# Performance work log

Measured on AMD Instinct MI355X. Metric: run time of the kernel, lower is better.

Reference implementation:

```python
import jax, jax.numpy as jnp
import numpy as np

OUT_F, IN_F = 4096, 11008
NUMEL = OUT_F * IN_F            # divisible by 256
NUM_SUPER = NUMEL // 256        # super-blocks of 8 sub-blocks x 32 values


def setup_inputs() -> dict:
    key = jax.random.key(0)
    k = jax.random.split(key, 7)
    x = jax.random.normal(k[0], (64, IN_F), dtype=jnp.float32)
    packed = jax.random.randint(k[1], (NUMEL // 2,), 0, 256, dtype=jnp.int32)
    d = jax.random.uniform(k[2], (NUM_SUPER,), dtype=jnp.float32) * 0.02
    dmin = jax.random.uniform(k[3], (NUM_SUPER,), dtype=jnp.float32) * 0.02
    scales = jax.random.randint(k[4], (NUM_SUPER * 8,), 0, 64, dtype=jnp.int32)
    mins = jax.random.randint(k[5], (NUM_SUPER * 8,), 0, 64, dtype=jnp.int32)
    bias = jax.random.normal(k[6], (OUT_F,), dtype=jnp.float32) * 0.02
    return {"x": x, "packed": packed, "d": d, "dmin": dmin,
            "scales": scales, "mins": mins, "bias": bias}


def _dequant_q4k(packed, d, dmin, scales, mins):
    # unpack two 4-bit quants per byte, interleaved low/high (stack dim=1 + flatten)
    low = packed & 15
    high = (packed >> 4) & 15
    q = jnp.stack([low, high], axis=1).reshape(NUM_SUPER, 8, 32).astype(jnp.float32)
    sc = (scales.astype(jnp.float32) / 63.0).reshape(NUM_SUPER, 8, 1)
    mn = (mins.astype(jnp.float32) / 63.0).reshape(NUM_SUPER, 8, 1)
    normalized = q / 15.0 * sc + mn
    w = normalized * d.reshape(NUM_SUPER, 1, 1) + dmin.reshape(NUM_SUPER, 1, 1)
    return w.reshape(OUT_F, IN_F)


def reference(x, packed, d, dmin, scales, mins, bias):
    w = _dequant_q4k(packed, d, dmin, scales, mins)   # [OUT_F, IN_F] fp32
    return x @ w.T + bias                              # F.linear
```

## Files before the change

### kernel.cpp

```cpp
#include <hip/hip_runtime.h>
#include <stdint.h>

#define OUT_F   4096
#define IN_F    11008
#define BATCH   64
#define NSUP    43
#define SB_ROW  344
#define IPR     5504
#define NKS     16
#define NCB     32
#define XP_BYTES   (344 * 256 * 16)
#define SCMN_BYTES (NSUP * 4096 * 16)
#define DDM_BYTES  (NSUP * 4096 * 8)
#define PART_OFF   (XP_BYTES + SCMN_BYTES + DDM_BYTES)
#define PART_BYTES ((size_t)NKS * BATCH * OUT_F * 4)
#define WS_FULL    (PART_OFF + PART_BYTES)

typedef __attribute__((ext_vector_type(8))) short  short8;
typedef __attribute__((ext_vector_type(4))) float  floatx4;
typedef __attribute__((ext_vector_type(4))) int    intx4;

__device__ __forceinline__ unsigned pack_bf16(float f0, float f1) {
    return __builtin_amdgcn_perm(__float_as_uint(f1), __float_as_uint(f0), 0x07060302u);
}

__global__ __launch_bounds__(256) void prep_kernel(const float* __restrict__ x,
                                                   const int* __restrict__ scales,
                                                   const int* __restrict__ mins,
                                                   const float* __restrict__ dd,
                                                   const float* __restrict__ dmn,
                                                   intx4* __restrict__ xp,
                                                   intx4* __restrict__ scmn_p,
                                                   float2* __restrict__ ddm_p) {
    if (blockIdx.x < 344) {
        const int ksb = blockIdx.x;
        const int mt  = threadIdx.x >> 6;
        const int l   = threadIdx.x & 63;
        const int lo  = l & 15, hi = l >> 4;
        const float* src = x + (mt * 16 + lo) * IN_F + ksb * 32 + hi * 8;
        floatx4 a0 = *(const floatx4*)src;
        floatx4 a1 = *(const floatx4*)(src + 4);
        intx4 r;
        r.x = pack_bf16(a0.x, a0.y);
        r.y = pack_bf16(a0.z, a0.w);
        r.z = pack_bf16(a1.x, a1.y);
        r.w = pack_bf16(a1.z, a1.w);
        xp[(mt * 344 + ksb) * 64 + l] = r;
    } else {
        const int tg  = (blockIdx.x - 344) * 256 + threadIdx.x;
        const int row = tg / 43;
        const int sup = tg - row * 43;
        const intx4 s0 = *(const intx4*)(scales + row * SB_ROW + sup * 8);
        const intx4 s1 = *(const intx4*)(scales + row * SB_ROW + sup * 8 + 4);
        const intx4 m0 = *(const intx4*)(mins   + row * SB_ROW + sup * 8);
        const intx4 m1 = *(const intx4*)(mins   + row * SB_ROW + sup * 8 + 4);
        intx4 o;
        o.x = s0.x | (s0.y << 8) | (s0.z << 16) | (s0.w << 24);
        o.y = s1.x | (s1.y << 8) | (s1.z << 16) | (s1.w << 24);
        o.z = m0.x | (m0.y << 8) | (m0.z << 16) | (m0.w << 24);
        o.w = m1.x | (m1.y << 8) | (m1.z << 16) | (m1.w << 24);
        scmn_p[sup * 4096 + row] = o;
        float2 dp;
        dp.x = dd[row * NSUP + sup];
        dp.y = dmn[row * NSUP + sup];
        ddm_p[sup * 4096 + row] = dp;
    }
}

__global__ __launch_bounds__(256) void init_out_kernel(const float* __restrict__ bias,
                                                       float* __restrict__ out) {
    int i = blockIdx.x * 256 + threadIdx.x;
    out[i] = bias[i & (OUT_F - 1)];
}

__global__ __launch_bounds__(256) void reduce_kernel(const float* __restrict__ part,
                                                     const float* __restrict__ bias,
                                                     float* __restrict__ out) {
    const int i = blockIdx.x * 256 + threadIdx.x;
    float s = bias[i & (OUT_F - 1)];
    #pragma unroll
    for (int k = 0; k < NKS; ++k) s += part[(size_t)k * (BATCH * OUT_F) + i];
    out[i] = s;
}

template<bool USE_PART>
__global__ __launch_bounds__(256, 2) void qlin_main(
    const intx4*  __restrict__ xp,
    const int*    __restrict__ packed,
    const intx4*  __restrict__ scmn_p,
    const float2* __restrict__ ddm_p,
    float*        __restrict__ part,
    float*        __restrict__ out)
{
    __shared__ intx4  xfs[2][2048];
    __shared__ intx4  scs[2][128];
    __shared__ float2 dds[2][128];

    const int ks  = blockIdx.x & 15;
    const int nb  = blockIdx.x >> 4;
    const int tid = threadIdx.x;
    const int w   = tid >> 6;
    const int l   = tid & 63;
    const int lo  = l & 15, hi = l >> 4;

    const int sup0 = ks < 11 ? 3 * ks : 33 + 2 * (ks - 11);
    const int nsup = ks < 11 ? 3 : 2;

    const int o0 = nb * 128 + (2 * w) * 16 + lo;
    const int o1 = o0 + 16;
    const int* bpA0 = packed + o0 * IPR + hi * 4;
    const int* bpA1 = packed + o1 * IPR + hi * 4;

    floatx4 acc[4][2];
    #pragma unroll
    for (int mt = 0; mt < 4; ++mt) { acc[mt][0] = (floatx4)0.0f; acc[mt][1] = (floatx4)0.0f; }

    auto stage = [&](int sup, int b) {
        intx4 xtmp[8];
        const intx4* xsrc = xp + sup * 512;
        #pragma unroll
        for (int i = 0; i < 8; ++i) {
            const int idx = i * 256 + tid;
            xtmp[i] = xsrc[(idx >> 9) * 22016 + (idx & 511)];
        }
        intx4 sctv; float2 ddv;
        if (tid < 128) sctv = scmn_p[sup * 4096 + nb * 128 + tid];
        else           ddv  = ddm_p[sup * 4096 + nb * 128 + (tid - 128)];
        #pragma unroll
        for (int i = 0; i < 8; ++i) xfs[b][i * 256 + tid] = xtmp[i];
        if (tid < 128) scs[b][tid] = sctv;
        else           dds[b][tid - 128] = ddv;
    };

    struct Half { intx4 v[2][4]; };
    auto load_half = [&](int sup, int half) {
        Half r;
        #pragma unroll
        for (int st = 0; st < 4; ++st) {
            r.v[0][st] = *(const intx4*)(bpA0 + sup * 128 + half * 64 + st * 16);
            r.v[1][st] = *(const intx4*)(bpA1 + sup * 128 + half * 64 + st * 16);
        }
        return r;
    };

    stage(sup0, 0);
    Half brP = load_half(sup0, 0);

    #pragma unroll 1
    for (int s = 0; s < nsup; ++s) {
        const int b = s & 1;
        const int sup = sup0 + s;
        __syncthreads();

        if (s + 1 < nsup) stage(sup + 1, 1 - b);
        Half brQ = load_half(sup, 1);

        const intx4  sv0 = scs[b][w * 32 + lo];
        const intx4  sv1 = scs[b][w * 32 + 16 + lo];
        const float2 dp0 = dds[b][w * 32 + lo];
        const float2 dp1 = dds[b][w * 32 + 16 + lo];
        const float a945_0 = dp0.x * (1.0f / 945.0f), a63_0 = dp0.x * (1.0f / 63.0f);
        const float a945_1 = dp1.x * (1.0f / 945.0f), a63_1 = dp1.x * (1.0f / 63.0f);

        auto compute_half = [&](int half, const Half& br) {
            #pragma unroll
            for (int st = 0; st < 4; ++st) {
                const int step = half * 4 + st;
                intx4 x0 = xfs[b][0 * 512 + step * 64 + l];
                intx4 x1 = xfs[b][1 * 512 + step * 64 + l];
                intx4 x2 = xfs[b][2 * 512 + step * 64 + l];
                intx4 x3 = xfs[b][3 * 512 + step * 64 + l];
                #pragma unroll
                for (int nt = 0; nt < 2; ++nt) {
                    const intx4 sv = nt ? sv1 : sv0;
                    const int scw = half ? sv.y : sv.x;
                    const int mnw = half ? sv.w : sv.z;
                    const float A = (nt ? a945_1 : a945_0) * (float)((scw >> (st * 8)) & 255);
                    const float B = fmaf((nt ? a63_1 : a63_0),
                                         (float)((mnw >> (st * 8)) & 255),
                                         (nt ? dp1.y : dp0.y));
                    const intx4 bv = br.v[nt][st];
                    union { intx4 i; short8 s8; } uw;
                    uw.i.x = pack_bf16(fmaf((float)(bv.x & 15), A, B),
                                       fmaf((float)(bv.x >> 4), A, B));
                    uw.i.y = pack_bf16(fmaf((float)(bv.y & 15), A, B),
                                       fmaf((float)(bv.y >> 4), A, B));
                    uw.i.z = pack_bf16(fmaf((float)(bv.z & 15), A, B),
                                       fmaf((float)(bv.z >> 4), A, B));
                    uw.i.w = pack_bf16(fmaf((float)(bv.w & 15), A, B),
                                       fmaf((float)(bv.w >> 4), A, B));
                    union { intx4 i; short8 s8; } u0, u1, u2, u3;
                    u0.i = x0; u1.i = x1; u2.i = x2; u3.i = x3;
                    acc[0][nt] = __builtin_amdgcn_mfma_f32_16x16x32_bf16(u0.s8, uw.s8, acc[0][nt], 0, 0, 0);
                    acc[1][nt] = __builtin_amdgcn_mfma_f32_16x16x32_bf16(u1.s8, uw.s8, acc[1][nt], 0, 0, 0);
                    acc[2][nt] = __builtin_amdgcn_mfma_f32_16x16x32_bf16(u2.s8, uw.s8, acc[2][nt], 0, 0, 0);
                    acc[3][nt] = __builtin_amdgcn_mfma_f32_16x16x32_bf16(u3.s8, uw.s8, acc[3][nt], 0, 0, 0);
                }
            }
        };

        compute_half(0, brP);
        if (s + 1 < nsup) brP = load_half(sup + 1, 0);
        compute_half(1, brQ);
    }

    if (USE_PART) {
        float* p0 = part + (size_t)ks * (BATCH * OUT_F);
        #pragma unroll
        for (int mt = 0; mt < 4; ++mt) {
            #pragma unroll
            for (int r = 0; r < 4; ++r) {
                const int row = (mt * 16 + hi * 4 + r) * OUT_F;
                p0[row + o0] = acc[mt][0][r];
                p0[row + o1] = acc[mt][1][r];
            }
        }
    } else {
        #pragma unroll
        for (int mt = 0; mt < 4; ++mt) {
            #pragma unroll
            for (int r = 0; r < 4; ++r) {
                const int row = (mt * 16 + hi * 4 + r) * OUT_F;
                atomicAdd(out + row + o0, acc[mt][0][r]);
                atomicAdd(out + row + o1, acc[mt][1][r]);
            }
        }
    }
}

extern "C" void kernel_launch(void* const* d_in, const int* in_sizes, int n_in,
                              void* d_out, int out_size, void* d_ws, size_t ws_size,
                              hipStream_t stream) {
    (void)in_sizes; (void)n_in; (void)out_size;
    const float* x      = (const float*)d_in[0];
    const int*   packed = (const int*)d_in[1];
    const float* d      = (const float*)d_in[2];
    const float* dmin   = (const float*)d_in[3];
    const int*   scales = (const int*)d_in[4];
    const int*   mins   = (const int*)d_in[5];
    const float* bias   = (const float*)d_in[6];
    float* out = (float*)d_out;

    intx4*  xp     = (intx4*)d_ws;
    intx4*  scmn_p = (intx4*)((char*)d_ws + XP_BYTES);
    float2* ddm_p  = (float2*)((char*)d_ws + XP_BYTES + SCMN_BYTES);
    float*  part   = (float*)((char*)d_ws + PART_OFF);
    const bool has_part = ws_size >= (size_t)WS_FULL;

    prep_kernel<<<344 + 688, 256, 0, stream>>>(x, scales, mins, d, dmin, xp, scmn_p, ddm_p);

    if (has_part) {
        qlin_main<true><<<NCB * NKS, 256, 0, stream>>>(
            xp, packed, scmn_p, ddm_p, part, out);
        reduce_kernel<<<(BATCH * OUT_F) / 256, 256, 0, stream>>>(part, bias, out);
    } else {
        init_out_kernel<<<(BATCH * OUT_F) / 256, 256, 0, stream>>>(bias, out);
        qlin_main<false><<<NCB * NKS, 256, 0, stream>>>(
            xp, packed, scmn_p, ddm_p, part, out);
    }
}
```

Baseline: 173.8 us.

## Stage packed weights through LDS with coalesced loads and halve output tile per block

Weight quants are now loaded cooperatively with coalesced row-chunk loads into a padded LDS tile, replacing per-lane strided register loads from global memory. Each block covers 64 output rows instead of 128 across 8 K-splits instead of 16, which raises the block count per split and lengthens each block's K range. The double-buffered prefetch pipeline is removed in favour of a simple load, sync, compute loop. This gives up overlap of memory and compute and adds an extra barrier plus LDS traffic, in exchange for better global coalescing.

```diff
diff --git a/kernel.cpp b/kernel.cpp
--- a/kernel.cpp
+++ b/kernel.cpp
@@ -7,8 +7,8 @@
 #define NSUP    43
 #define SB_ROW  344
 #define IPR     5504
-#define NKS     16
-#define NCB     32
+#define NKS     8
+#define NCB     64
 #define XP_BYTES   (344 * 256 * 16)
 #define SCMN_BYTES (NSUP * 4096 * 16)
 #define DDM_BYTES  (NSUP * 4096 * 8)
@@ -92,30 +92,42 @@
     float*        __restrict__ part,
     float*        __restrict__ out)
 {
-    __shared__ intx4  xfs[2][2048];
-    __shared__ intx4  scs[2][128];
-    __shared__ float2 dds[2][128];
-
-    const int ks  = blockIdx.x & 15;
-    const int nb  = blockIdx.x >> 4;
+    __shared__ int    wds[64 * 132];
+    __shared__ intx4  xfs[2048];
+    __shared__ intx4  scs[64];
+    __shared__ float2 dds[64];
+
+    const int ks  = blockIdx.x & 7;
+    const int nb  = blockIdx.x >> 3;
     const int tid = threadIdx.x;
     const int w   = tid >> 6;
     const int l   = tid & 63;
     const int lo  = l & 15, hi = l >> 4;
 
-    const int sup0 = ks < 11 ? 3 * ks : 33 + 2 * (ks - 11);
-    const int nsup = ks < 11 ? 3 : 2;
-
-    const int o0 = nb * 128 + (2 * w) * 16 + lo;
-    const int o1 = o0 + 16;
-    const int* bpA0 = packed + o0 * IPR + hi * 4;
-    const int* bpA1 = packed + o1 * IPR + hi * 4;
-
-    floatx4 acc[4][2];
+    const int sup0 = ks < 3 ? 6 * ks : 18 + 5 * (ks - 3);
+    const int nsup = ks < 3 ? 6 : 5;
+
+    const int srow = w * 16 + (l >> 5);
+    const int schk = l & 31;
+    const int* gb0 = packed + (nb * 64 + srow) * IPR + schk * 4;
+
+    floatx4 acc[4];
     #pragma unroll
-    for (int mt = 0; mt < 4; ++mt) { acc[mt][0] = (floatx4)0.0f; acc[mt][1] = (floatx4)0.0f; }
-
-    auto stage = [&](int sup, int b) {
+    for (int mt = 0; mt < 4; ++mt) acc[mt] = (floatx4)0.0f;
+
+    const int myrow = w * 16 + lo;
+
+    #pragma unroll 1
+    for (int s = 0; s < nsup; ++s) {
+        const int sup = sup0 + s;
+        __syncthreads();
+
+        intx4 wtmp[8];
+        const int* gb = gb0 + sup * 128;
+        #pragma unroll
+        for (int i = 0; i < 8; ++i)
+            wtmp[i] = *(const intx4*)(gb + 2 * i * IPR);
+
         intx4 xtmp[8];
         const intx4* xsrc = xp + sup * 512;
         #pragma unroll
@@ -124,106 +136,69 @@
             xtmp[i] = xsrc[(idx >> 9) * 22016 + (idx & 511)];
         }
         intx4 sctv; float2 ddv;
-        if (tid < 128) sctv = scmn_p[sup * 4096 + nb * 128 + tid];
-        else           ddv  = ddm_p[sup * 4096 + nb * 128 + (tid - 128)];
-        #pragma unroll
-        for (int i = 0; i < 8; ++i) xfs[b][i * 256 + tid] = xtmp[i];
-        if (tid < 128) scs[b][tid] = sctv;
-        else           dds[b][tid - 128] = ddv;
-    };
-
-    struct Half { intx4 v[2][4]; };
-    auto load_half = [&](int sup, int half) {
-        Half r;
-        #pragma unroll
-        for (int st = 0; st < 4; ++st) {
-            r.v[0][st] = *(const intx4*)(bpA0 + sup * 128 + half * 64 + st * 16);
-            r.v[1][st] = *(const intx4*)(bpA1 + sup * 128 + half * 64 + st * 16);
-        }
-        return r;
-    };
-
-    stage(sup0, 0);
-    Half brP = load_half(sup0, 0);
-
-    #pragma unroll 1
-    for (int s = 0; s < nsup; ++s) {
-        const int b = s & 1;
-        const int sup = sup0 + s;
+        if (tid < 64)       sctv = scmn_p[sup * 4096 + nb * 64 + tid];
+        else if (tid < 128) ddv  = ddm_p[sup * 4096 + nb * 64 + (tid - 64)];
+
+        #pragma unroll
+        for (int i = 0; i < 8; ++i)
+            *(intx4*)&wds[(srow + 2 * i) * 132 + schk * 4] = wtmp[i];
+        #pragma unroll
+        for (int i = 0; i < 8; ++i)
+            xfs[i * 256 + tid] = xtmp[i];
+        if (tid < 64)       scs[tid] = sctv;
+        else if (tid < 128) dds[tid - 64] = ddv;
         __syncthreads();
 
-        if (s + 1 < nsup) stage(sup + 1, 1 - b);
-        Half brQ = load_half(sup, 1);
-
-        const intx4  sv0 = scs[b][w * 32 + lo];
-        const intx4  sv1 = scs[b][w * 32 + 16 + lo];
-        const float2 dp0 = dds[b][w * 32 + lo];
-        const float2 dp1 = dds[b][w * 32 + 16 + lo];
-        const float a945_0 = dp0.x * (1.0f / 945.0f), a63_0 = dp0.x * (1.0f / 63.0f);
-        const float a945_1 = dp1.x * (1.0f / 945.0f), a63_1 = dp1.x * (1.0f / 63.0f);
-
-        auto compute_half = [&](int half, const Half& br) {
-            #pragma unroll
-            for (int st = 0; st < 4; ++st) {
-                const int step = half * 4 + st;
-                intx4 x0 = xfs[b][0 * 512 + step * 64 + l];
-                intx4 x1 = xfs[b][1 * 512 + step * 64 + l];
-                intx4 x2 = xfs[b][2 * 512 + step * 64 + l];
-                intx4 x3 = xfs[b][3 * 512 + step * 64 + l];
-                #pragma unroll
-                for (int nt = 0; nt < 2; ++nt) {
-                    const intx4 sv = nt ? sv1 : sv0;
-                    const int scw = half ? sv.y : sv.x;
-                    const int mnw = half ? sv.w : sv.z;
-                    const float A = (nt ? a945_1 : a945_0) * (float)((scw >> (st * 8)) & 255);
-                    const float B = fmaf((nt ? a63_1 : a63_0),
-                                         (float)((mnw >> (st * 8)) & 255),
-                                         (nt ? dp1.y : dp0.y));
-                    const intx4 bv = br.v[nt][st];
-                    union { intx4 i; short8 s8; } uw;
-                    uw.i.x = pack_bf16(fmaf((float)(bv.x & 15), A, B),
-                                       fmaf((float)(bv.x >> 4), A, B));
-                    uw.i.y = pack_bf16(fmaf((float)(bv.y & 15), A, B),
-                                       fmaf((float)(bv.y >> 4), A, B));
-                    uw.i.z = pack_bf16(fmaf((float)(bv.z & 15), A, B),
-                                       fmaf((float)(bv.z >> 4), A, B));
-                    uw.i.w = pack_bf16(fmaf((float)(bv.w & 15), A, B),
-                                       fmaf((float)(bv.w >> 4), A, B));
-                    union { intx4 i; short8 s8; } u0, u1, u2, u3;
-                    u0.i = x0; u1.i = x1; u2.i = x2; u3.i = x3;
-                    acc[0][nt] = __builtin_amdgcn_mfma_f32_16x16x32_bf16(u0.s8, uw.s8, acc[0][nt], 0, 0, 0);
-                    acc[1][nt] = __builtin_amdgcn_mfma_f32_16x16x32_bf16(u1.s8, uw.s8, acc[1][nt], 0, 0, 0);
-                    acc[2][nt] = __builtin_amdgcn_mfma_f32_16x16x32_bf16(u2.s8, uw.s8, acc[2][nt], 0, 0, 0);
-                    acc[3][nt] = __builtin_amdgcn_mfma_f32_16x16x32_bf16(u3.s8, uw.s8, acc[3][nt], 0, 0, 0);
-                }
-            }
-        };
-
-        compute_half(0, brP);
-        if (s + 1 < nsup) brP = load_half(sup + 1, 0);
-        compute_half(1, brQ);
-    }
-
+        const intx4  sv = scs[myrow];
+        const float2 dp = dds[myrow];
+        const float a945 = dp.x * (1.0f / 945.0f);
+        const float a63  = dp.x * (1.0f / 63.0f);
+
+        #pragma unroll
+        for (int st = 0; st < 8; ++st) {
+            const intx4 bv = *(const intx4*)&wds[myrow * 132 + st * 16 + hi * 4];
+            const int scw = (st < 4) ? sv.x : sv.y;
+            const int mnw = (st < 4) ? sv.z : sv.w;
+            const float A = a945 * (float)((scw >> ((st & 3) * 8)) & 255);
+            const float B = fmaf(a63, (float)((mnw >> ((st & 3) * 8)) & 255), dp.y);
+
+            union { intx4 i; short8 s8; } uw;
+            uw.i.x = pack_bf16(fmaf((float)(bv.x & 15), A, B),
+                               fmaf((float)(bv.x >> 4), A, B));
+            uw.i.y = pack_bf16(fmaf((float)(bv.y & 15), A, B),
+                               fmaf((float)(bv.y >> 4), A, B));
+            uw.i.z = pack_bf16(fmaf((float)(bv.z & 15), A, B),
+                               fmaf((float)(bv.z >> 4), A, B));
+            uw.i.w = pack_bf16(fmaf((float)(bv.w & 15), A, B),
+                               fmaf((float)(bv.w >> 4), A, B));
+
+            union { intx4 i; short8 s8; } u0, u1, u2, u3;
+            u0.i = xfs[0 * 512 + st * 64 + l];
+            u1.i = xfs[1 * 512 + st * 64 + l];
+            u2.i = xfs[2 * 512 + st * 64 + l];
+            u3.i = xfs[3 * 512 + st * 64 + l];
+            acc[0] = __builtin_amdgcn_mfma_f32_16x16x32_bf16(u0.s8, uw.s8, acc[0], 0, 0, 0);
+            acc[1] = __builtin_amdgcn_mfma_f32_16x16x32_bf16(u1.s8, uw.s8, acc[1], 0, 0, 0);
+            acc[2] = __builtin_amdgcn_mfma_f32_16x16x32_bf16(u2.s8, uw.s8, acc[2], 0, 0, 0);
+            acc[3] = __builtin_amdgcn_mfma_f32_16x16x32_bf16(u3.s8, uw.s8, acc[3], 0, 0, 0);
+        }
+    }
+
+    const int o = nb * 64 + myrow;
     if (USE_PART) {
-        float* p0 = part + (size_t)ks * (BATCH * OUT_F);
+        float* p0 = part + (size_t)ks * (BATCH * OUT_F) + o;
         #pragma unroll
         for (int mt = 0; mt < 4; ++mt) {
             #pragma unroll
-            for (int r = 0; r < 4; ++r) {
-                const int row = (mt * 16 + hi * 4 + r) * OUT_F;
-                p0[row + o0] = acc[mt][0][r];
-                p0[row + o1] = acc[mt][1][r];
-            }
+            for (int r = 0; r < 4; ++r)
+                p0[(mt * 16 + hi * 4 + r) * OUT_F] = acc[mt][r];
         }
     } else {
         #pragma unroll
         for (int mt = 0; mt < 4; ++mt) {
             #pragma unroll
-            for (int r = 0; r < 4; ++r) {
-                const int row = (mt * 16 + hi * 4 + r) * OUT_F;
-                atomicAdd(out + row + o0, acc[mt][0][r]);
-                atomicAdd(out + row + o1, acc[mt][1][r]);
-            }
+            for (int r = 0; r < 4; ++r)
+                atomicAdd(out + (mt * 16 + hi * 4 + r) * OUT_F + o, acc[mt][r]);
         }
     }
 }
```

Result: faster. 169.8 us (-2.3%).
